# Kernel tuning notes

Hardware: AMD Instinct MI355X
Metric: run time of the kernel (lower is better)

The kernel has to match this reference:

```python
import jax, jax.numpy as jnp
import numpy as np

B, N, D = 8, 4096, 512
K = 1228  # int(4096 * 0.3)
N_CH = 2


def setup_inputs() -> dict:
    key = jax.random.key(0)
    ks = jax.random.split(key, 6)
    return {
        "agents_states": jax.random.normal(ks[0], (B, N, D), jnp.float32),
        "net": jax.random.normal(ks[1], (N_CH, N, N), jnp.float32) * (1.0 / np.sqrt(N)),
        "gate_w": jax.random.normal(ks[2], (N_CH, D, 2 * D), jnp.float32) * 0.02,
        "gate_b": jnp.zeros((N_CH, D), jnp.float32),
        "cand_w": jax.random.normal(ks[3], (N_CH, D, D), jnp.float32) * 0.02,
        "cand_b": jnp.zeros((N_CH, D), jnp.float32),
        "ln_g": jnp.ones((N_CH, D), jnp.float32),
        "ln_b": jnp.zeros((N_CH, D), jnp.float32),
        "channel_mix": jnp.ones((N_CH,), jnp.float32) / N_CH,
        "k": K,
    }


def _layer_norm(h, g, b, eps=1e-5):
    mu = h.mean(-1, keepdims=True)
    var = jnp.mean((h - mu) ** 2, axis=-1, keepdims=True)
    return (h - mu) * jax.lax.rsqrt(var + eps) * g + b


def _channel(x, net, gw, gb, cw, cb, lg, lb):
    # fixed-graph message passing: [N,N] @ [B,N,D]
    interaction = jnp.einsum('mn,bnd->bmd', net, x)
    candidate = jax.nn.gelu(interaction @ cw.T + cb, approximate=False)
    gate = jax.nn.sigmoid(jnp.concatenate([x, interaction], axis=-1) @ gw.T + gb)
    return _layer_norm(gate * candidate + (1.0 - gate) * x, lg, lb)


def reference(agents_states, net, gate_w, gate_b, cand_w, cand_b, ln_g, ln_b, channel_mix, k):
    w = jax.nn.softmax(channel_mix, axis=0)
    out = jnp.zeros_like(agents_states)
    for c in range(net.shape[0]):  # fixed small channel count
        out = out + w[c] * _channel(agents_states, net[c], gate_w[c], gate_b[c],
                                    cand_w[c], cand_b[c], ln_g[c], ln_b[c])
    # sparse top-k activation over agents
    energy = jnp.linalg.norm(out, axis=-1)               # [B, N]
    _, top_idx = jax.lax.top_k(energy, k)                # [B, k]
    mask = jnp.zeros_like(energy).at[jnp.arange(energy.shape[0])[:, None], top_idx].set(1.0)
    mask = mask * (out.shape[1] / k)
    return out * mask[..., None]
```

## Files before the change

kernel.cpp:

```cpp
#include <hip/hip_runtime.h>
#include <hip/hip_bf16.h>
#include <math.h>

#define BB 8
#define NN 4096
#define DD 512
#define SLAB 2048
#define SROWS (BB * SLAB)

typedef short bf16x8 __attribute__((ext_vector_type(8)));
typedef float f32x4 __attribute__((ext_vector_type(4)));

#define AS1 __attribute__((address_space(1)))
#define AS3 __attribute__((address_space(3)))

__device__ __forceinline__ void gload_lds16(const void* g, void* l) {
    __builtin_amdgcn_global_load_lds((const AS1 unsigned int*)g,
                                     (AS3 unsigned int*)l, 16, 0, 0);
}

__device__ __forceinline__ void split_bf16(float v, unsigned short& h, unsigned short& l) {
    __hip_bfloat16 bh = __float2bfloat16(v);
    float hf = __bfloat162float(bh);
    __hip_bfloat16 bl = __float2bfloat16(v - hf);
    h = *reinterpret_cast<unsigned short*>(&bh);
    l = *reinterpret_cast<unsigned short*>(&bl);
}

__global__ __launch_bounds__(256)
void conv_split(const float* __restrict__ src, unsigned short* __restrict__ hi,
                unsigned short* __restrict__ lo)
{
    const size_t i = (size_t)blockIdx.x * 256 + threadIdx.x;
    float4 v = ((const float4*)src)[i];
    ushort4 h, l;
    split_bf16(v.x, h.x, l.x);
    split_bf16(v.y, h.y, l.y);
    split_bf16(v.z, h.z, l.z);
    split_bf16(v.w, h.w, l.w);
    ((ushort4*)hi)[i] = h;
    ((ushort4*)lo)[i] = l;
}

__global__ __launch_bounds__(256)
void conv_w3(const float* __restrict__ cw, const float* __restrict__ gw,
             unsigned short* __restrict__ cwh, unsigned short* __restrict__ cwl,
             unsigned short* __restrict__ gxh, unsigned short* __restrict__ gxl,
             unsigned short* __restrict__ gih, unsigned short* __restrict__ gil)
{
    const int blk = blockIdx.x;
    const int i = (blk & 255) * 256 + threadIdx.x;
    const int n = i >> 7, kq = (i & 127) * 4;
    const float* src;
    unsigned short *oh, *ol;
    if (blk < 256)      { src = cw + (size_t)n * 512 + kq;        oh = cwh; ol = cwl; }
    else if (blk < 512) { src = gw + (size_t)n * 1024 + kq;       oh = gxh; ol = gxl; }
    else                { src = gw + (size_t)n * 1024 + 512 + kq; oh = gih; ol = gil; }
    float4 v = *(const float4*)src;
    ushort4 h, l;
    split_bf16(v.x, h.x, l.x);
    split_bf16(v.y, h.y, l.y);
    split_bf16(v.z, h.z, l.z);
    split_bf16(v.w, h.w, l.w);
    *(ushort4*)(oh + (size_t)n * 512 + kq) = h;
    *(ushort4*)(ol + (size_t)n * 512 + kq) = l;
}

__global__ __launch_bounds__(256)
void conv_xs(const float* __restrict__ x, int nbase,
             unsigned short* __restrict__ hi, unsigned short* __restrict__ lo)
{
    const size_t i = (size_t)blockIdx.x * 256 + threadIdx.x;
    const int r = (int)(i >> 7), kq = (int)(i & 127) * 4;
    const int b = r >> 11, ii = r & (SLAB - 1);
    float4 v = *(const float4*)(x + ((size_t)(b << 12) + nbase + ii) * DD + kq);
    ushort4 h, l;
    split_bf16(v.x, h.x, l.x);
    split_bf16(v.y, h.y, l.y);
    split_bf16(v.z, h.z, l.z);
    split_bf16(v.w, h.w, l.w);
    *(ushort4*)(hi + (size_t)r * DD + kq) = h;
    *(ushort4*)(lo + (size_t)r * DD + kq) = l;
}

__global__ __launch_bounds__(256)
void conv_xT(const float* __restrict__ x, unsigned short* __restrict__ th,
             unsigned short* __restrict__ tl)
{
    __shared__ unsigned short Th[64][65];
    __shared__ unsigned short Tl[64][65];
    const int n0 = blockIdx.x * 64, d0 = blockIdx.y * 64, b = blockIdx.z;
    const int t = threadIdx.x;
    const int r = t >> 4, c4 = (t & 15) * 4;
#pragma unroll
    for (int i = 0; i < 4; ++i) {
        int row = r + i * 16;
        float4 v = *(const float4*)(x + ((size_t)b * NN + n0 + row) * DD + d0 + c4);
        split_bf16(v.x, Th[row][c4 + 0], Tl[row][c4 + 0]);
        split_bf16(v.y, Th[row][c4 + 1], Tl[row][c4 + 1]);
        split_bf16(v.z, Th[row][c4 + 2], Tl[row][c4 + 2]);
        split_bf16(v.w, Th[row][c4 + 3], Tl[row][c4 + 3]);
    }
    __syncthreads();
    const int od = t >> 2;
    const int on0 = (t & 3) * 16;
    unsigned short hb[16], lb[16];
#pragma unroll
    for (int j = 0; j < 16; ++j) { hb[j] = Th[on0 + j][od]; lb[j] = Tl[on0 + j][od]; }
    const size_t obase = ((size_t)b * DD + d0 + od) * (size_t)NN + n0 + on0;
#pragma unroll
    for (int q = 0; q < 4; ++q) {
        ushort4 hv = {hb[q * 4 + 0], hb[q * 4 + 1], hb[q * 4 + 2], hb[q * 4 + 3]};
        ushort4 lv = {lb[q * 4 + 0], lb[q * 4 + 1], lb[q * 4 + 2], lb[q * 4 + 3]};
        *(ushort4*)(th + obase + q * 4) = hv;
        *(ushort4*)(tl + obase + q * 4) = lv;
    }
}

__global__ __launch_bounds__(256, 2)
void gemm_big(const unsigned short* __restrict__ Ah, const unsigned short* __restrict__ Al,
              const unsigned short* __restrict__ Bh, const unsigned short* __restrict__ Bl,
              unsigned short* __restrict__ Ch, unsigned short* __restrict__ Cl)
{
    __shared__ alignas(16) unsigned short sAh[128 * 32];
    __shared__ alignas(16) unsigned short sAl[128 * 32];
    __shared__ alignas(16) unsigned short sBh[128 * 32];
    __shared__ alignas(16) unsigned short sBl[128 * 32];

    const int tid = threadIdx.x;
    const int lane = tid & 63;
    const int w = tid >> 6;

    const int n0 = blockIdx.x * 128;
    const int b  = blockIdx.y;
    const int m0 = blockIdx.z * 128;

    Bh += (size_t)b * DD * NN;
    Bl += (size_t)b * DD * NN;

    const int c0 = w * 2, c1 = c0 + 1;
    const int u2 = lane >> 2;
    const int sst = (u2 + (u2 >> 2)) & 3;
    const int kc = (lane & 3) ^ sst;
    const size_t gA0 = (size_t)(m0 + c0 * 16 + u2) * NN + kc * 8;
    const size_t gA1 = (size_t)(m0 + c1 * 16 + u2) * NN + kc * 8;
    const size_t gB0 = (size_t)(n0 + c0 * 16 + u2) * NN + kc * 8;
    const size_t gB1 = (size_t)(n0 + c1 * 16 + u2) * NN + kc * 8;
    unsigned short* lAh0 = sAh + c0 * 512; unsigned short* lAh1 = sAh + c1 * 512;
    unsigned short* lAl0 = sAl + c0 * 512; unsigned short* lAl1 = sAl + c1 * 512;
    unsigned short* lBh0 = sBh + c0 * 512; unsigned short* lBh1 = sBh + c1 * 512;
    unsigned short* lBl0 = sBl + c0 * 512; unsigned short* lBl1 = sBl + c1 * 512;

    const int wm = (w & 1) * 64, wn = (w >> 1) * 64;
    const int fr = lane & 15;
    const int sf = (fr + (fr >> 2)) & 3;
    const int fslot = ((lane >> 4) ^ sf) * 16;
    int offA[4], offB[4];
#pragma unroll
    for (int i = 0; i < 4; ++i) {
        offA[i] = (wm + i * 16 + fr) * 64 + fslot;
        offB[i] = (wn + i * 16 + fr) * 64 + fslot;
    }

    f32x4 acc[4][4] = {};

    for (int kt = 0; kt < NN; kt += 32) {
        __syncthreads();
        gload_lds16(Ah + gA0 + kt, lAh0);
        gload_lds16(Ah + gA1 + kt, lAh1);
        gload_lds16(Al + gA0 + kt, lAl0);
        gload_lds16(Al + gA1 + kt, lAl1);
        gload_lds16(Bh + gB0 + kt, lBh0);
        gload_lds16(Bh + gB1 + kt, lBh1);
        gload_lds16(Bl + gB0 + kt, lBl0);
        gload_lds16(Bl + gB1 + kt, lBl1);
        asm volatile("s_waitcnt vmcnt(0)" ::: "memory");
        __syncthreads();

        bf16x8 ah[4], al[4], bh[4], bl[4];
#pragma unroll
        for (int i = 0; i < 4; ++i) {
            ah[i] = *(const bf16x8*)((const char*)sAh + offA[i]);
            al[i] = *(const bf16x8*)((const char*)sAl + offA[i]);
            bh[i] = *(const bf16x8*)((const char*)sBh + offB[i]);
            bl[i] = *(const bf16x8*)((const char*)sBl + offB[i]);
        }
#pragma unroll
        for (int mi = 0; mi < 4; ++mi)
#pragma unroll
            for (int ni = 0; ni < 4; ++ni) {
                acc[mi][ni] = __builtin_amdgcn_mfma_f32_16x16x32_bf16(al[mi], bh[ni], acc[mi][ni], 0, 0, 0);
                acc[mi][ni] = __builtin_amdgcn_mfma_f32_16x16x32_bf16(ah[mi], bl[ni], acc[mi][ni], 0, 0, 0);
                acc[mi][ni] = __builtin_amdgcn_mfma_f32_16x16x32_bf16(ah[mi], bh[ni], acc[mi][ni], 0, 0, 0);
            }
    }

    const int erow = (lane >> 4) * 4;
#pragma unroll
    for (int mi = 0; mi < 4; ++mi)
#pragma unroll
        for (int ni = 0; ni < 4; ++ni) {
            const int r0 = m0 + wm + mi * 16 + erow;
            const int col = n0 + wn + ni * 16 + fr;
#pragma unroll
            for (int r = 0; r < 4; ++r) {
                unsigned short h, l;
                split_bf16(acc[mi][ni][r], h, l);
                const size_t idx = ((size_t)b * SLAB + r0 + r) * DD + col;
                Ch[idx] = h;
                Cl[idx] = l;
            }
        }
}

__global__ __launch_bounds__(256, 2)
void gemm_small(const unsigned short* __restrict__ Ah, const unsigned short* __restrict__ Al,
                const unsigned short* __restrict__ Bh, const unsigned short* __restrict__ Bl,
                const float* __restrict__ bias, float* __restrict__ C, int accum)
{
    __shared__ alignas(16) unsigned short sAh[128 * 32];
    __shared__ alignas(16) unsigned short sAl[128 * 32];
    __shared__ alignas(16) unsigned short sBh[128 * 32];
    __shared__ alignas(16) unsigned short sBl[128 * 32];

    const int tid = threadIdx.x;
    const int lane = tid & 63;
    const int w = tid >> 6;

    const int n0 = blockIdx.x * 128;
    const int m0 = blockIdx.y * 128;

    const int c0 = w * 2, c1 = c0 + 1;
    const int u2 = lane >> 2;
    const int sst = (u2 + (u2 >> 2)) & 3;
    const int kc = (lane & 3) ^ sst;
    const size_t gA0 = (size_t)(m0 + c0 * 16 + u2) * DD + kc * 8;
    const size_t gA1 = (size_t)(m0 + c1 * 16 + u2) * DD + kc * 8;
    const size_t gB0 = (size_t)(n0 + c0 * 16 + u2) * DD + kc * 8;
    const size_t gB1 = (size_t)(n0 + c1 * 16 + u2) * DD + kc * 8;
    unsigned short* lAh0 = sAh + c0 * 512; unsigned short* lAh1 = sAh + c1 * 512;
    unsigned short* lAl0 = sAl + c0 * 512; unsigned short* lAl1 = sAl + c1 * 512;
    unsigned short* lBh0 = sBh + c0 * 512; unsigned short* lBh1 = sBh + c1 * 512;
    unsigned short* lBl0 = sBl + c0 * 512; unsigned short* lBl1 = sBl + c1 * 512;

    const int wm = (w & 1) * 64, wn = (w >> 1) * 64;
    const int fr = lane & 15;
    const int sf = (fr + (fr >> 2)) & 3;
    const int fslot = ((lane >> 4) ^ sf) * 16;
    int offA[4], offB[4];
#pragma unroll
    for (int i = 0; i < 4; ++i) {
        offA[i] = (wm + i * 16 + fr) * 64 + fslot;
        offB[i] = (wn + i * 16 + fr) * 64 + fslot;
    }

    f32x4 acc[4][4] = {};

    for (int kt = 0; kt < DD; kt += 32) {
        __syncthreads();
        gload_lds16(Ah + gA0 + kt, lAh0);
        gload_lds16(Ah + gA1 + kt, lAh1);
        gload_lds16(Al + gA0 + kt, lAl0);
        gload_lds16(Al + gA1 + kt, lAl1);
        gload_lds16(Bh + gB0 + kt, lBh0);
        gload_lds16(Bh + gB1 + kt, lBh1);
        gload_lds16(Bl + gB0 + kt, lBl0);
        gload_lds16(Bl + gB1 + kt, lBl1);
        asm volatile("s_waitcnt vmcnt(0)" ::: "memory");
        __syncthreads();

        bf16x8 ah[4], al[4], bh[4], bl[4];
#pragma unroll
        for (int i = 0; i < 4; ++i) {
            ah[i] = *(const bf16x8*)((const char*)sAh + offA[i]);
            al[i] = *(const bf16x8*)((const char*)sAl + offA[i]);
            bh[i] = *(const bf16x8*)((const char*)sBh + offB[i]);
            bl[i] = *(const bf16x8*)((const char*)sBl + offB[i]);
        }
#pragma unroll
        for (int mi = 0; mi < 4; ++mi)
#pragma unroll
            for (int ni = 0; ni < 4; ++ni) {
                acc[mi][ni] = __builtin_amdgcn_mfma_f32_16x16x32_bf16(al[mi], bh[ni], acc[mi][ni], 0, 0, 0);
                acc[mi][ni] = __builtin_amdgcn_mfma_f32_16x16x32_bf16(ah[mi], bl[ni], acc[mi][ni], 0, 0, 0);
                acc[mi][ni] = __builtin_amdgcn_mfma_f32_16x16x32_bf16(ah[mi], bh[ni], acc[mi][ni], 0, 0, 0);
            }
    }

    const int erow = (lane >> 4) * 4;
#pragma unroll
    for (int mi = 0; mi < 4; ++mi)
#pragma unroll
        for (int ni = 0; ni < 4; ++ni) {
            const int r0 = m0 + wm + mi * 16 + erow;
            const int col = n0 + wn + ni * 16 + fr;
            const float bv = bias ? bias[col] : 0.0f;
#pragma unroll
            for (int r = 0; r < 4; ++r) {
                const size_t idx = (size_t)(r0 + r) * DD + col;
                float v = acc[mi][ni][r] + bv;
                if (accum) v += C[idx];
                C[idx] = v;
            }
        }
}

__global__ __launch_bounds__(128)
void pw_slab(const float* __restrict__ x, const float* __restrict__ gp_,
             const float* __restrict__ cp_, const float* __restrict__ lg,
             const float* __restrict__ lb, const float* __restrict__ cmix,
             int c, int nbase, float* __restrict__ out, float* __restrict__ energy)
{
    __shared__ float sm[4];
    const int rloc = blockIdx.x;
    const int b = rloc >> 11, ii = rloc & (SLAB - 1);
    const int grow = (b << 12) + nbase + ii;
    const int tid = threadIdx.x;
    const size_t lbase = (size_t)rloc * DD + tid * 4;
    const size_t gbase = (size_t)grow * DD + tid * 4;

    float4 g4 = *(const float4*)(gp_ + lbase);
    float4 c4 = *(const float4*)(cp_ + lbase);
    float4 x4 = *(const float4*)(x + gbase);
    float gv[4] = {g4.x, g4.y, g4.z, g4.w};
    float cv[4] = {c4.x, c4.y, c4.z, c4.w};
    float xv[4] = {x4.x, x4.y, x4.z, x4.w};
    float h[4];
#pragma unroll
    for (int j = 0; j < 4; ++j) {
        float gate = 1.0f / (1.0f + expf(-gv[j]));
        float cand = 0.5f * cv[j] * (1.0f + erff(cv[j] * 0.70710678118654752440f));
        h[j] = gate * cand + (1.0f - gate) * xv[j];
    }

    const int lane = tid & 63, wid = tid >> 6;
    float s = h[0] + h[1] + h[2] + h[3];
#pragma unroll
    for (int off = 32; off > 0; off >>= 1) s += __shfl_xor(s, off, 64);
    if (lane == 0) sm[wid] = s;
    __syncthreads();
    float mu = (sm[0] + sm[1]) * (1.0f / 512.0f);
    float vs = 0.0f;
#pragma unroll
    for (int j = 0; j < 4; ++j) { float d = h[j] - mu; vs += d * d; }
#pragma unroll
    for (int off = 32; off > 0; off >>= 1) vs += __shfl_xor(vs, off, 64);
    if (lane == 0) sm[2 + wid] = vs;
    __syncthreads();
    float var = (sm[2] + sm[3]) * (1.0f / 512.0f);
    float rstd = 1.0f / sqrtf(var + 1e-5f);

    float m0 = cmix[0], m1 = cmix[1];
    float mx = fmaxf(m0, m1);
    float e0 = expf(m0 - mx), e1 = expf(m1 - mx);
    float wgt = ((c == 0) ? e0 : e1) / (e0 + e1);

    const int dix = tid * 4;
    float4 lg4 = *(const float4*)(lg + dix);
    float4 lb4 = *(const float4*)(lb + dix);
    float lgv[4] = {lg4.x, lg4.y, lg4.z, lg4.w};
    float lbv[4] = {lb4.x, lb4.y, lb4.z, lb4.w};
    float ov[4];
    if (c == 0) {
#pragma unroll
        for (int j = 0; j < 4; ++j)
            ov[j] = wgt * ((h[j] - mu) * rstd * lgv[j] + lbv[j]);
    } else {
        float4 o4 = *(const float4*)(out + gbase);
        ov[0] = o4.x; ov[1] = o4.y; ov[2] = o4.z; ov[3] = o4.w;
#pragma unroll
        for (int j = 0; j < 4; ++j)
            ov[j] += wgt * ((h[j] - mu) * rstd * lgv[j] + lbv[j]);
    }
    float4 st = {ov[0], ov[1], ov[2], ov[3]};
    *(float4*)(out + gbase) = st;

    if (c == 1) {
        float s2 = ov[0] * ov[0] + ov[1] * ov[1] + ov[2] * ov[2] + ov[3] * ov[3];
#pragma unroll
        for (int off = 32; off > 0; off >>= 1) s2 += __shfl_xor(s2, off, 64);
        __syncthreads();
        if (lane == 0) sm[wid] = s2;
        __syncthreads();
        if (tid == 0) energy[grow] = sqrtf(sm[0] + sm[1]);
    }
}

__global__ __launch_bounds__(1024)
void topk_kernel(float* __restrict__ energy, const int* __restrict__ kptr)
{
    __shared__ unsigned keys[NN];
    __shared__ int hist[256];
    __shared__ int wsum[16];
    __shared__ unsigned sh_pfx;
    __shared__ int sh_need;

    const int b = blockIdx.x, tid = threadIdx.x;
    float* e = energy + (size_t)b * NN;
    for (int n = tid; n < NN; n += 1024) keys[n] = __float_as_uint(e[n]);
    const int K = *kptr;
    if (tid == 0) { sh_pfx = 0u; sh_need = K; }
    __syncthreads();

    for (int round = 0; round < 4; ++round) {
        const int shift = 24 - 8 * round;
        if (tid < 256) hist[tid] = 0;
        __syncthreads();
        const unsigned pfx = sh_pfx;
        const unsigned mhi = (round == 0) ? 0u : (0xFFFFFFFFu << (shift + 8));
        for (int n = tid; n < NN; n += 1024) {
            unsigned kv = keys[n];
            if ((kv & mhi) == pfx) atomicAdd(&hist[(kv >> shift) & 255], 1);
        }
        __syncthreads();
        if (tid == 0) {
            int need = sh_need;
            int d = 255;
            for (;; --d) {
                int cct = hist[d];
                if (need <= cct) break;
                need -= cct;
            }
            sh_pfx = pfx | ((unsigned)d << shift);
            sh_need = need;
        }
        __syncthreads();
    }

    const unsigned T = sh_pfx;
    const int need = sh_need;

    const int n0 = tid * 4;
    unsigned kv[4]; int eq[4]; int loc[4];
    int s = 0;
#pragma unroll
    for (int j = 0; j < 4; ++j) {
        kv[j] = keys[n0 + j];
        eq[j] = (kv[j] == T) ? 1 : 0;
        loc[j] = s; s += eq[j];
    }
    const int lane = tid & 63, wid = tid >> 6;
    int v = s;
#pragma unroll
    for (int off = 1; off < 64; off <<= 1) {
        int u = __shfl_up(v, off, 64);
        if (lane >= off) v += u;
    }
    if (lane == 63) wsum[wid] = v;
    __syncthreads();
    if (tid == 0) {
        int acc = 0;
        for (int w2 = 0; w2 < 16; ++w2) { int t = wsum[w2]; wsum[w2] = acc; acc += t; }
    }
    __syncthreads();
    const int base = wsum[wid] + (v - s);
    const float scale = (float)(4096.0 / (double)K);
#pragma unroll
    for (int j = 0; j < 4; ++j) {
        bool sel = (kv[j] > T) || (eq[j] && (base + loc[j]) < need);
        e[n0 + j] = sel ? scale : 0.0f;
    }
}

__global__ __launch_bounds__(128)
void mask_kernel(float* __restrict__ out, const float* __restrict__ mscale)
{
    const int row = blockIdx.x;
    const int tid = threadIdx.x;
    const size_t base = (size_t)row * DD + tid * 4;
    const float sc = mscale[row];
    float4 v = *(const float4*)(out + base);
    v.x *= sc; v.y *= sc; v.z *= sc; v.w *= sc;
    *(float4*)(out + base) = v;
}

extern "C" void kernel_launch(void* const* d_in, const int* in_sizes, int n_in,
                              void* d_out, int out_size, void* d_ws, size_t ws_size,
                              hipStream_t stream)
{
    const float* x      = (const float*)d_in[0];
    const float* net    = (const float*)d_in[1];
    const float* gate_w = (const float*)d_in[2];
    const float* gate_b = (const float*)d_in[3];
    const float* cand_w = (const float*)d_in[4];
    const float* cand_b = (const float*)d_in[5];
    const float* ln_g   = (const float*)d_in[6];
    const float* ln_b   = (const float*)d_in[7];
    const float* cmix   = (const float*)d_in[8];
    const int*   kptr   = (const int*)d_in[9];
    float* out = (float*)d_out;

    const size_t ROWS  = (size_t)BB * NN;
    const size_t PLANE = ROWS * DD;

    char* p = (char*)d_ws;
    unsigned short* xTh = (unsigned short*)p;             p += PLANE * 2;
    unsigned short* xTl = (unsigned short*)p;             p += PLANE * 2;
    char* slotN = p;                                      p += (size_t)SLAB * NN * 2 * 2;
    unsigned short* netsh = (unsigned short*)slotN;
    unsigned short* netsl = netsh + (size_t)SLAB * NN;
    unsigned short* cwh = (unsigned short*)slotN;
    unsigned short* cwl = cwh + 512 * 512;
    unsigned short* gxh = cwl + 512 * 512;
    unsigned short* gxl = gxh + 512 * 512;
    unsigned short* gih = gxl + 512 * 512;
    unsigned short* gil = gih + 512 * 512;
    unsigned short* inth = (unsigned short*)p;            p += (size_t)SROWS * DD * 2;
    unsigned short* intl = (unsigned short*)p;            p += (size_t)SROWS * DD * 2;
    char* slotX = p;                                      p += (size_t)SROWS * DD * 4;
    unsigned short* xsh = (unsigned short*)slotX;
    unsigned short* xsl = xsh + (size_t)SROWS * DD;
    float* candp = (float*)slotX;
    float* gatep = (float*)p;                             p += (size_t)SROWS * DD * 4;
    float* energy = (float*)p;

    conv_xT<<<dim3(NN / 64, DD / 64, BB), 256, 0, stream>>>(x, xTh, xTl);

    for (int c = 0; c < 2; ++c) {
        for (int s = 0; s < 2; ++s) {
            const int nbase = s * SLAB;
            conv_split<<<(SLAB * NN / 4) / 256, 256, 0, stream>>>(
                net + (size_t)c * NN * NN + (size_t)nbase * NN, netsh, netsl);
            gemm_big<<<dim3(DD / 128, BB, SLAB / 128), 256, 0, stream>>>(
                netsh, netsl, xTh, xTl, inth, intl);
            conv_w3<<<768, 256, 0, stream>>>(
                cand_w + (size_t)c * DD * DD, gate_w + (size_t)c * DD * 2 * DD,
                cwh, cwl, gxh, gxl, gih, gil);
            conv_xs<<<(SROWS * DD / 4) / 256, 256, 0, stream>>>(x, nbase, xsh, xsl);
            gemm_small<<<dim3(4, SROWS / 128), 256, 0, stream>>>(
                xsh, xsl, gxh, gxl, gate_b + (size_t)c * DD, gatep, 0);
            gemm_small<<<dim3(4, SROWS / 128), 256, 0, stream>>>(
                inth, intl, cwh, cwl, cand_b + (size_t)c * DD, candp, 0);
            gemm_small<<<dim3(4, SROWS / 128), 256, 0, stream>>>(
                inth, intl, gih, gil, nullptr, gatep, 1);
            pw_slab<<<SROWS, 128, 0, stream>>>(
                x, gatep, candp, ln_g + (size_t)c * DD, ln_b + (size_t)c * DD,
                cmix, c, nbase, out, energy);
        }
    }

    topk_kernel<<<BB, 1024, 0, stream>>>(energy, kptr);
    mask_kernel<<<(int)ROWS, 128, 0, stream>>>(out, energy);
}
```

Measured before the change: 1.728 ms.

## Use 2-wave 64x128 warp tiles in big GEMM and fuse gate GEMMs over concatenated K

The big message-passing GEMM now runs 128-thread blocks in which each wave owns a 64x128 output tile instead of 64x64. B fragments are loaded once per ni and reused across four M fragments, which cuts LDS reads per MFMA. Separately, the two gate GEMMs (x part and interaction part) are fused into one launch that walks a concatenated K of 1024. This drops a launch and the read-modify-write accumulate pass on the gate buffer. In exchange, the warp-tile change doubles accumulator registers per thread (128 floats) and halves the waves per block, which risks lower occupancy and less latency hiding.

Measured after the change: 1.974 ms. 1.14x slower.

```diff
diff --git a/kernel.cpp b/kernel.cpp
--- a/kernel.cpp
+++ b/kernel.cpp
@@ -117,7 +117,7 @@
     }
 }
 
-__global__ __launch_bounds__(256, 2)
+__global__ __launch_bounds__(128, 2)
 void gemm_big(const unsigned short* __restrict__ Ah, const unsigned short* __restrict__ Al,
               const unsigned short* __restrict__ Bh, const unsigned short* __restrict__ Bl,
               unsigned short* __restrict__ Ch, unsigned short* __restrict__ Cl)
@@ -138,70 +138,69 @@
     Bh += (size_t)b * DD * NN;
     Bl += (size_t)b * DD * NN;
 
-    const int c0 = w * 2, c1 = c0 + 1;
     const int u2 = lane >> 2;
     const int sst = (u2 + (u2 >> 2)) & 3;
     const int kc = (lane & 3) ^ sst;
-    const size_t gA0 = (size_t)(m0 + c0 * 16 + u2) * NN + kc * 8;
-    const size_t gA1 = (size_t)(m0 + c1 * 16 + u2) * NN + kc * 8;
-    const size_t gB0 = (size_t)(n0 + c0 * 16 + u2) * NN + kc * 8;
-    const size_t gB1 = (size_t)(n0 + c1 * 16 + u2) * NN + kc * 8;
-    unsigned short* lAh0 = sAh + c0 * 512; unsigned short* lAh1 = sAh + c1 * 512;
-    unsigned short* lAl0 = sAl + c0 * 512; unsigned short* lAl1 = sAl + c1 * 512;
-    unsigned short* lBh0 = sBh + c0 * 512; unsigned short* lBh1 = sBh + c1 * 512;
-    unsigned short* lBl0 = sBl + c0 * 512; unsigned short* lBl1 = sBl + c1 * 512;
-
-    const int wm = (w & 1) * 64, wn = (w >> 1) * 64;
+    unsigned gAo[4], gBo[4];
+#pragma unroll
+    for (int i = 0; i < 4; ++i) {
+        const int c = w * 4 + i;
+        gAo[i] = (unsigned)((m0 + c * 16 + u2) * NN + kc * 8);
+        gBo[i] = (unsigned)((n0 + c * 16 + u2) * NN + kc * 8);
+    }
+
+    const int wm = w * 64;
     const int fr = lane & 15;
+    const int kg = lane >> 4;
     const int sf = (fr + (fr >> 2)) & 3;
-    const int fslot = ((lane >> 4) ^ sf) * 16;
-    int offA[4], offB[4];
-#pragma unroll
-    for (int i = 0; i < 4; ++i) {
-        offA[i] = (wm + i * 16 + fr) * 64 + fslot;
-        offB[i] = (wn + i * 16 + fr) * 64 + fslot;
-    }
-
-    f32x4 acc[4][4] = {};
+    const int fslot = (kg ^ sf) * 16;
+    int offA[4], offB[8];
+#pragma unroll
+    for (int i = 0; i < 4; ++i) offA[i] = (wm + i * 16 + fr) * 64 + fslot;
+#pragma unroll
+    for (int i = 0; i < 8; ++i) offB[i] = (i * 16 + fr) * 64 + fslot;
+
+    f32x4 acc[4][8] = {};
 
     for (int kt = 0; kt < NN; kt += 32) {
         __syncthreads();
-        gload_lds16(Ah + gA0 + kt, lAh0);
-        gload_lds16(Ah + gA1 + kt, lAh1);
-        gload_lds16(Al + gA0 + kt, lAl0);
-        gload_lds16(Al + gA1 + kt, lAl1);
-        gload_lds16(Bh + gB0 + kt, lBh0);
-        gload_lds16(Bh + gB1 + kt, lBh1);
-        gload_lds16(Bl + gB0 + kt, lBl0);
-        gload_lds16(Bl + gB1 + kt, lBl1);
+#pragma unroll
+        for (int i = 0; i < 4; ++i) {
+            const int lo = (w * 4 + i) * 512;
+            gload_lds16(Ah + gAo[i] + kt, sAh + lo);
+            gload_lds16(Al + gAo[i] + kt, sAl + lo);
+            gload_lds16(Bh + gBo[i] + kt, sBh + lo);
+            gload_lds16(Bl + gBo[i] + kt, sBl + lo);
+        }
         asm volatile("s_waitcnt vmcnt(0)" ::: "memory");
         __syncthreads();
 
-        bf16x8 ah[4], al[4], bh[4], bl[4];
+        bf16x8 ah[4], al[4];
 #pragma unroll
         for (int i = 0; i < 4; ++i) {
             ah[i] = *(const bf16x8*)((const char*)sAh + offA[i]);
             al[i] = *(const bf16x8*)((const char*)sAl + offA[i]);
-            bh[i] = *(const bf16x8*)((const char*)sBh + offB[i]);
-            bl[i] = *(const bf16x8*)((const char*)sBl + offB[i]);
-        }
-#pragma unroll
-        for (int mi = 0; mi < 4; ++mi)
-#pragma unroll
-            for (int ni = 0; ni < 4; ++ni) {
-                acc[mi][ni] = __builtin_amdgcn_mfma_f32_16x16x32_bf16(al[mi], bh[ni], acc[mi][ni], 0, 0, 0);
-                acc[mi][ni] = __builtin_amdgcn_mfma_f32_16x16x32_bf16(ah[mi], bl[ni], acc[mi][ni], 0, 0, 0);
-                acc[mi][ni] = __builtin_amdgcn_mfma_f32_16x16x32_bf16(ah[mi], bh[ni], acc[mi][ni], 0, 0, 0);
+        }
+#pragma unroll
+        for (int ni = 0; ni < 8; ++ni) {
+            bf16x8 bh = *(const bf16x8*)((const char*)sBh + offB[ni]);
+            bf16x8 bl = *(const bf16x8*)((const char*)sBl + offB[ni]);
+#pragma unroll
+            for (int mi = 0; mi < 4; ++mi) {
+                acc[mi][ni] = __builtin_amdgcn_mfma_f32_16x16x32_bf16(al[mi], bh, acc[mi][ni], 0, 0, 0);
+                acc[mi][ni] = __builtin_amdgcn_mfma_f32_16x16x32_bf16(ah[mi], bl, acc[mi][ni], 0, 0, 0);
+                acc[mi][ni] = __builtin_amdgcn_mfma_f32_16x16x32_bf16(ah[mi], bh, acc[mi][ni], 0, 0, 0);
             }
-    }
-
-    const int erow = (lane >> 4) * 4;
+        }
+    }
+
+    const int erow = kg * 4;
 #pragma unroll
     for (int mi = 0; mi < 4; ++mi)
 #pragma unroll
-        for (int ni = 0; ni < 4; ++ni) {
+        for (int ni = 0; ni < 8; ++ni) {
             const int r0 = m0 + wm + mi * 16 + erow;
-            const int col = n0 + wn + ni * 16 + fr;
+            const int col = n0 + ni * 16 + fr;
 #pragma unroll
             for (int r = 0; r < 4; ++r) {
                 unsigned short h, l;
@@ -214,9 +213,11 @@
 }
 
 __global__ __launch_bounds__(256, 2)
-void gemm_small(const unsigned short* __restrict__ Ah, const unsigned short* __restrict__ Al,
-                const unsigned short* __restrict__ Bh, const unsigned short* __restrict__ Bl,
-                const float* __restrict__ bias, float* __restrict__ C, int accum)
+void gemm_small(const unsigned short* __restrict__ A1h, const unsigned short* __restrict__ A1l,
+                const unsigned short* __restrict__ A2h, const unsigned short* __restrict__ A2l,
+                const unsigned short* __restrict__ B1h, const unsigned short* __restrict__ B1l,
+                const unsigned short* __restrict__ B2h, const unsigned short* __restrict__ B2l,
+                const float* __restrict__ bias, float* __restrict__ C, int Ktot)
 {
     __shared__ alignas(16) unsigned short sAh[128 * 32];
     __shared__ alignas(16) unsigned short sAl[128 * 32];
@@ -256,16 +257,21 @@
 
     f32x4 acc[4][4] = {};
 
-    for (int kt = 0; kt < DD; kt += 32) {
-        __syncthreads();
-        gload_lds16(Ah + gA0 + kt, lAh0);
-        gload_lds16(Ah + gA1 + kt, lAh1);
-        gload_lds16(Al + gA0 + kt, lAl0);
-        gload_lds16(Al + gA1 + kt, lAl1);
-        gload_lds16(Bh + gB0 + kt, lBh0);
-        gload_lds16(Bh + gB1 + kt, lBh1);
-        gload_lds16(Bl + gB0 + kt, lBl0);
-        gload_lds16(Bl + gB1 + kt, lBl1);
+    for (int kt = 0; kt < Ktot; kt += 32) {
+        const unsigned short* pAh = (kt < 512) ? A1h : A2h;
+        const unsigned short* pAl = (kt < 512) ? A1l : A2l;
+        const unsigned short* pBh = (kt < 512) ? B1h : B2h;
+        const unsigned short* pBl = (kt < 512) ? B1l : B2l;
+        const int ko = kt & 511;
+        __syncthreads();
+        gload_lds16(pAh + gA0 + ko, lAh0);
+        gload_lds16(pAh + gA1 + ko, lAh1);
+        gload_lds16(pAl + gA0 + ko, lAl0);
+        gload_lds16(pAl + gA1 + ko, lAl1);
+        gload_lds16(pBh + gB0 + ko, lBh0);
+        gload_lds16(pBh + gB1 + ko, lBh1);
+        gload_lds16(pBl + gB0 + ko, lBl0);
+        gload_lds16(pBl + gB1 + ko, lBl1);
         asm volatile("s_waitcnt vmcnt(0)" ::: "memory");
         __syncthreads();
 
@@ -294,13 +300,11 @@
         for (int ni = 0; ni < 4; ++ni) {
             const int r0 = m0 + wm + mi * 16 + erow;
             const int col = n0 + wn + ni * 16 + fr;
-            const float bv = bias ? bias[col] : 0.0f;
+            const float bv = bias[col];
 #pragma unroll
             for (int r = 0; r < 4; ++r) {
                 const size_t idx = (size_t)(r0 + r) * DD + col;
-                float v = acc[mi][ni][r] + bv;
-                if (accum) v += C[idx];
-                C[idx] = v;
+                C[idx] = acc[mi][ni][r] + bv;
             }
         }
 }
@@ -521,18 +525,18 @@
             const int nbase = s * SLAB;
             conv_split<<<(SLAB * NN / 4) / 256, 256, 0, stream>>>(
                 net + (size_t)c * NN * NN + (size_t)nbase * NN, netsh, netsl);
-            gemm_big<<<dim3(DD / 128, BB, SLAB / 128), 256, 0, stream>>>(
+            gemm_big<<<dim3(DD / 128, BB, SLAB / 128), 128, 0, stream>>>(
                 netsh, netsl, xTh, xTl, inth, intl);
             conv_w3<<<768, 256, 0, stream>>>(
                 cand_w + (size_t)c * DD * DD, gate_w + (size_t)c * DD * 2 * DD,
                 cwh, cwl, gxh, gxl, gih, gil);
             conv_xs<<<(SROWS * DD / 4) / 256, 256, 0, stream>>>(x, nbase, xsh, xsl);
             gemm_small<<<dim3(4, SROWS / 128), 256, 0, stream>>>(
-                xsh, xsl, gxh, gxl, gate_b + (size_t)c * DD, gatep, 0);
+                xsh, xsl, inth, intl, gxh, gxl, gih, gil,
+                gate_b + (size_t)c * DD, gatep, 1024);
             gemm_small<<<dim3(4, SROWS / 128), 256, 0, stream>>>(
-                inth, intl, cwh, cwl, cand_b + (size_t)c * DD, candp, 0);
-            gemm_small<<<dim3(4, SROWS / 128), 256, 0, stream>>>(
-                inth, intl, gih, gil, nullptr, gatep, 1);
+                inth, intl, inth, intl, cwh, cwl, cwh, cwl,
+                cand_b + (size_t)c * DD, candp, 512);
             pw_slab<<<SROWS, 128, 0, stream>>>(
                 x, gatep, candp, ln_g + (size_t)c * DD, ln_b + (size_t)c * DD,
                 cmix, c, nbase, out, energy);
```
